# Kernel optimization log

Hardware: AMD Instinct MI355X
Metric: run time of the kernel (lower is better)

The kernel has to match this reference:

```python
import jax, jax.numpy as jnp
import numpy as np

NUM_ITERS = 3

def squash(s, axis=-1):
    # standard capsule squash: ||s||^2/(1+||s||^2) * s/||s||
    sq = jnp.sum(s * s, axis=axis, keepdims=True)
    norm = jnp.sqrt(sq)
    return (sq / (1.0 + sq)) * (s / norm)

def setup_inputs() -> dict:
    key = jax.random.key(0)
    kx, kw = jax.random.split(key)
    B, I, k, l, O = 512, 1152, 8, 16, 7
    x = jax.random.normal(kx, (B, I, k), dtype=jnp.float32)
    w = jax.random.normal(kw, (I, k, l, O), dtype=jnp.float32)
    return {"x": x, "w": w}

def reference(x, w):
    # x: [B, I, k]; w: [I, k, l, O]
    u_hat = jnp.einsum('BIk,IklO->BIlO', x, w)            # [B, I, l, O]
    I, _, l, _ = w.shape
    b_ij = jnp.zeros((I, l), dtype=u_hat.dtype)
    v_j = None
    for _ in range(NUM_ITERS):
        c_ij = jax.nn.softmax(b_ij, axis=0)               # softmax over I
        s_j = jnp.einsum('Il,BIlO->BlO', c_ij, u_hat)     # [B, l, O]
        v_j = jnp.transpose(squash(s_j), (0, 2, 1))       # [B, O, l]
        u_vj = jnp.einsum('BOl,BIlO->BIl', v_j, u_hat).mean(axis=0)  # [I, l]
        b_ij = b_ij + u_vj
    return v_j
```

## Files before the change

### kernel.cpp

```cpp
#include <hip/hip_runtime.h>
#include <hip/hip_bf16.h>


#define NB 512
#define NI 1152
#define NLO 112
#define NIK 9216
#define NPAD 128

typedef __attribute__((ext_vector_type(8))) short bf16x8;
typedef __attribute__((ext_vector_type(4))) float f32x4;

__device__ __forceinline__ ushort f2bf(float f) {
    __hip_bfloat16 h = __float2bfloat16(f);
    return *(ushort*)&h;
}
__device__ __forceinline__ float bf2f(short s) {
    union { unsigned int u; float f; } v;
    v.u = ((unsigned int)(unsigned short)s) << 16;
    return v.f;
}

__device__ __forceinline__ void conv_x_body(const float* __restrict__ x,
                                            ushort* __restrict__ xbf,
                                            ushort* __restrict__ xT, int bid) {
    __shared__ ushort tile[64][68];
    int kg = bid % 144, bg = bid / 144;
    int k0 = kg * 64, b0 = bg * 64;
    int t = threadIdx.x;
    for (int e = t; e < 1024; e += 256) {
        int r = e >> 4, c4 = (e & 15) * 4;
        float4 f = *(const float4*)&x[(size_t)(b0 + r) * NIK + k0 + c4];
        ushort4 u = { f2bf(f.x), f2bf(f.y), f2bf(f.z), f2bf(f.w) };
        *(ushort4*)&xbf[(size_t)(b0 + r) * NIK + k0 + c4] = u;
        tile[r][c4] = u.x; tile[r][c4 + 1] = u.y; tile[r][c4 + 2] = u.z; tile[r][c4 + 3] = u.w;
    }
    __syncthreads();
    for (int e = t; e < 1024; e += 256) {
        int kr = e >> 4, c4 = (e & 15) * 4;
        ushort4 u = { tile[c4][kr], tile[c4 + 1][kr], tile[c4 + 2][kr], tile[c4 + 3][kr] };
        *(ushort4*)&xT[(size_t)(k0 + kr) * NB + b0 + c4] = u;
    }
}

__global__ __launch_bounds__(256) void prep0(const float* __restrict__ x,
                                             ushort* __restrict__ xbf,
                                             ushort* __restrict__ xT,
                                             const float* __restrict__ w,
                                             ushort* __restrict__ wpT,
                                             ushort* __restrict__ wps,
                                             float* __restrict__ Z) {
    if (blockIdx.x < 1152) { conv_x_body(x, xbf, xT, blockIdx.x); return; }
    __shared__ ushort tile[NPAD][66];
    int t = threadIdx.x;
    int wb = blockIdx.x - 1152;
    int ik0 = wb * 64;
    if (blockIdx.x == 1152 && t < 48) Z[t] = (t < 16) ? 1152.0f : 0.0f;
    for (int e = t; e < 8192; e += 256) {
        int ikl = e >> 7, np = e & 127;
        int l = np >> 3, o = np & 7;
        float wv = (o < 7) ? w[(size_t)(ik0 + ikl) * NLO + l * 7 + o] : 0.f;
        tile[np][ikl] = f2bf(wv);
    }
    __syncthreads();
    for (int e = t; e < 8192; e += 256) {
        int np = e >> 6, ikl = e & 63;
        ushort v = tile[np][ikl];
        wpT[(size_t)np * NIK + ik0 + ikl] = v;
        wps[(size_t)np * NIK + ik0 + ikl] = v;
    }
}

__global__ __launch_bounds__(1024) void sq_gemm(const ushort* __restrict__ xbf,
                                                const ushort* __restrict__ wps,
                                                const float* __restrict__ Zit,
                                                ushort* __restrict__ vT,
                                                float* __restrict__ out, int wout) {
    __shared__ float sp[16][16][16];
    __shared__ float ss[16][16];
    __shared__ float facs[16][2];
    __shared__ float zi[2];
    int bid = blockIdx.x;
    int mt = bid & 31, ng = bid >> 5;
    int b0 = mt * 16, n0 = ng * 16;
    int t = threadIdx.x;
    int wv = t >> 6, lane = t & 63;
    int row = lane & 15, quad = lane >> 4;
    int k0 = wv * 576;
    if (t < 2) zi[t] = 1.0f / Zit[ng * 2 + t];
    const ushort* ap = xbf + (size_t)(b0 + row) * NIK + k0 + quad * 8;
    const ushort* bp = wps + (size_t)(n0 + row) * NIK + k0 + quad * 8;
    f32x4 acc = {0.f, 0.f, 0.f, 0.f};
    #pragma unroll
    for (int ks = 0; ks < 18; ++ks) {
        bf16x8 a = *(const bf16x8*)(ap + ks * 32);
        bf16x8 b = *(const bf16x8*)(bp + ks * 32);
        acc = __builtin_amdgcn_mfma_f32_16x16x32_bf16(a, b, acc, 0, 0, 0);
    }
    #pragma unroll
    for (int r = 0; r < 4; ++r) sp[wv][quad * 4 + r][row] = acc[r];
    __syncthreads();
    if (t < 256) {
        int m = t >> 4, n = t & 15;
        float sv = 0.f;
        #pragma unroll
        for (int w8 = 0; w8 < 16; ++w8) sv += sp[w8][m][n];
        ss[m][n] = sv * zi[n >> 3];
    }
    __syncthreads();
    if (t < 32) {
        int m = t >> 1, ll = t & 1;
        float sq = 0.f;
        #pragma unroll
        for (int o = 0; o < 8; ++o) { float e = ss[m][ll * 8 + o]; sq += e * e; }
        facs[m][ll] = sqrtf(sq) / (1.0f + sq);
    }
    __syncthreads();
    if (t < 256) {
        int m = t >> 4, n = t & 15;
        int o = n & 7, lg = ng * 2 + (n >> 3);
        if (o < 7) {
            float vv = ss[m][n] * facs[m][n >> 3];
            vT[(size_t)(o * 16 + lg) * NB + b0 + m] = f2bf(vv);
            if (wout) out[(size_t)(b0 + m) * NLO + o * 16 + lg] = vv;
        }
    }
}

__global__ __launch_bounds__(512) void g_wc(const ushort* __restrict__ xT,
                                            const ushort* __restrict__ vT,
                                            const float* __restrict__ w,
                                            float* __restrict__ bij,
                                            const ushort* __restrict__ wpT,
                                            ushort* __restrict__ wps,
                                            float* __restrict__ Zit, int accum) {
    __shared__ float bs[2][8][16];
    __shared__ float cs[128];
    int t = threadIdx.x;
    int wv = t >> 6;
    int lane = t & 63;
    int half = wv & 1;
    int mt = wv >> 1;
    int m0 = blockIdx.x * 64 + mt * 16;
    int kb0 = half * 256;
    int row = lane & 15, quad = lane >> 4;
    const ushort* ap = xT + (size_t)(m0 + row) * NB + kb0 + quad * 8;
    const ushort* bp = vT + (size_t)row * NB + kb0 + quad * 8;
    f32x4 acc[7];
    #pragma unroll
    for (int nt = 0; nt < 7; ++nt) acc[nt] = (f32x4){0.f, 0.f, 0.f, 0.f};
    #pragma unroll
    for (int ks = 0; ks < 8; ++ks) {
        bf16x8 a = *(const bf16x8*)(ap + ks * 32);
        #pragma unroll
        for (int nt = 0; nt < 7; ++nt) {
            bf16x8 bfr = *(const bf16x8*)(bp + (size_t)nt * 16 * NB + ks * 32);
            acc[nt] = __builtin_amdgcn_mfma_f32_16x16x32_bf16(a, bfr, acc[nt], 0, 0, 0);
        }
    }
    float S = 0.f;
    #pragma unroll
    for (int r = 0; r < 4; ++r) {
        int ik = m0 + quad * 4 + r;
        const float* wr = w + (size_t)ik * NLO + row * 7;
        float p = 0.f;
        #pragma unroll
        for (int o = 0; o < 7; ++o) p += wr[o] * acc[o][r];
        S += p;
    }
    float Sp = __shfl_down(S, 16);
    if ((quad & 1) == 0)
        bs[half][mt * 2 + (quad >> 1)][row] = (S + Sp) * (1.0f / 512.0f);
    __syncthreads();
    if (t < 128) {
        int il = t >> 4, l = t & 15;
        int i = blockIdx.x * 8 + il;
        float val = bs[0][il][l] + bs[1][il][l];
        if (accum) val += bij[i * 16 + l];
        bij[i * 16 + l] = val;
        cs[t] = expf(val);
    }
    __syncthreads();
    if (t < 16) {
        float z = 0.f;
        #pragma unroll
        for (int j = 0; j < 8; ++j) z += cs[j * 16 + t];
        atomicAdd(&Zit[t], z);
    }
    int ik0 = blockIdx.x * 64;
    for (int e = t; e < 2048; e += 512) {
        int np = e >> 4, i4 = (e & 15) * 4;
        float sc = cs[(i4 >> 3) * 16 + (np >> 3)];
        ushort4 wv4 = *(const ushort4*)&wpT[(size_t)np * NIK + ik0 + i4];
        ushort4 o4 = { f2bf(bf2f((short)wv4.x) * sc), f2bf(bf2f((short)wv4.y) * sc),
                       f2bf(bf2f((short)wv4.z) * sc), f2bf(bf2f((short)wv4.w) * sc) };
        *(ushort4*)&wps[(size_t)np * NIK + ik0 + i4] = o4;
    }
}

extern "C" void kernel_launch(void* const* d_in, const int* in_sizes, int n_in,
                              void* d_out, int out_size, void* d_ws, size_t ws_size,
                              hipStream_t stream) {
    const float* x = (const float*)d_in[0];
    const float* w = (const float*)d_in[1];
    float* out = (float*)d_out;
    float* ws = (float*)d_ws;
    float*  f_bij  = ws;
    float*  f_Z    = f_bij + NI * 16;
    ushort* xbf    = (ushort*)(f_Z + 48);
    ushort* xT     = xbf + (size_t)NB * NIK;
    ushort* wpT    = xT + (size_t)NIK * NB;
    ushort* wps    = wpT + (size_t)NPAD * NIK;
    ushort* vT     = wps + (size_t)NPAD * NIK;
    prep0<<<1296, 256, 0, stream>>>(x, xbf, xT, w, wpT, wps, f_Z);
    for (int it = 0; it < 3; ++it) {
        sq_gemm<<<256, 1024, 0, stream>>>(xbf, wps, f_Z + it * 16, vT, out,
                                          it == 2 ? 1 : 0);
        if (it < 2)
            g_wc<<<144, 512, 0, stream>>>(xT, vT, w, f_bij, wpT, wps,
                                          f_Z + (it + 1) * 16, it);
    }
}
```

Baseline: 174.1 us.

## Fuse routing iterations into one cooperative kernel with grid-wide syncs

Replaces the five separate sq_gemm/g_wc launches with a single cooperative kernel that loops over the three routing iterations and uses grid.sync() between phases. The agreement GEMM phase now runs on 144 of the 256 blocks with 1024 threads, splitting K into four quarters instead of two. This removes per-launch overhead and gaps between small kernels, in exchange for grid-wide barrier cost and idle blocks during the agreement phase.

Measured after the change: 314.4 us. +80.6%, slower.

```diff
diff --git a/kernel.cpp b/kernel.cpp
--- a/kernel.cpp
+++ b/kernel.cpp
@@ -1,5 +1,8 @@
 #include <hip/hip_runtime.h>
 #include <hip/hip_bf16.h>
+#include <hip/hip_cooperative_groups.h>
+
+namespace cg = cooperative_groups;
 
 
 #define NB 512
@@ -71,130 +74,131 @@
     }
 }
 
-__global__ __launch_bounds__(1024) void sq_gemm(const ushort* __restrict__ xbf,
-                                                const ushort* __restrict__ wps,
-                                                const float* __restrict__ Zit,
-                                                ushort* __restrict__ vT,
-                                                float* __restrict__ out, int wout) {
+__global__ __launch_bounds__(1024, 4) void route(const ushort* __restrict__ xbf,
+                                                 ushort* __restrict__ wps,
+                                                 float* __restrict__ Z,
+                                                 ushort* __restrict__ vT,
+                                                 float* __restrict__ out,
+                                                 const ushort* __restrict__ xT,
+                                                 const float* __restrict__ w,
+                                                 float* __restrict__ bij,
+                                                 const ushort* __restrict__ wpT) {
+    cg::grid_group grid = cg::this_grid();
     __shared__ float sp[16][16][16];
     __shared__ float ss[16][16];
     __shared__ float facs[16][2];
     __shared__ float zi[2];
+    __shared__ float bs[4][8][16];
+    __shared__ float cs[128];
     int bid = blockIdx.x;
-    int mt = bid & 31, ng = bid >> 5;
-    int b0 = mt * 16, n0 = ng * 16;
     int t = threadIdx.x;
     int wv = t >> 6, lane = t & 63;
     int row = lane & 15, quad = lane >> 4;
+    int mt = bid & 31, ng = bid >> 5;
+    int b0 = mt * 16, n0 = ng * 16;
     int k0 = wv * 576;
-    if (t < 2) zi[t] = 1.0f / Zit[ng * 2 + t];
     const ushort* ap = xbf + (size_t)(b0 + row) * NIK + k0 + quad * 8;
     const ushort* bp = wps + (size_t)(n0 + row) * NIK + k0 + quad * 8;
-    f32x4 acc = {0.f, 0.f, 0.f, 0.f};
-    #pragma unroll
-    for (int ks = 0; ks < 18; ++ks) {
-        bf16x8 a = *(const bf16x8*)(ap + ks * 32);
-        bf16x8 b = *(const bf16x8*)(bp + ks * 32);
-        acc = __builtin_amdgcn_mfma_f32_16x16x32_bf16(a, b, acc, 0, 0, 0);
-    }
-    #pragma unroll
-    for (int r = 0; r < 4; ++r) sp[wv][quad * 4 + r][row] = acc[r];
-    __syncthreads();
-    if (t < 256) {
-        int m = t >> 4, n = t & 15;
-        float sv = 0.f;
+
+    for (int it = 0; it < 3; ++it) {
+        if (t < 2) zi[t] = 1.0f / Z[it * 16 + ng * 2 + t];
+        f32x4 acc = {0.f, 0.f, 0.f, 0.f};
         #pragma unroll
-        for (int w8 = 0; w8 < 16; ++w8) sv += sp[w8][m][n];
-        ss[m][n] = sv * zi[n >> 3];
-    }
-    __syncthreads();
-    if (t < 32) {
-        int m = t >> 1, ll = t & 1;
-        float sq = 0.f;
+        for (int ks = 0; ks < 18; ++ks) {
+            bf16x8 a = *(const bf16x8*)(ap + ks * 32);
+            bf16x8 b = *(const bf16x8*)(bp + ks * 32);
+            acc = __builtin_amdgcn_mfma_f32_16x16x32_bf16(a, b, acc, 0, 0, 0);
+        }
         #pragma unroll
-        for (int o = 0; o < 8; ++o) { float e = ss[m][ll * 8 + o]; sq += e * e; }
-        facs[m][ll] = sqrtf(sq) / (1.0f + sq);
-    }
-    __syncthreads();
-    if (t < 256) {
-        int m = t >> 4, n = t & 15;
-        int o = n & 7, lg = ng * 2 + (n >> 3);
-        if (o < 7) {
-            float vv = ss[m][n] * facs[m][n >> 3];
-            vT[(size_t)(o * 16 + lg) * NB + b0 + m] = f2bf(vv);
-            if (wout) out[(size_t)(b0 + m) * NLO + o * 16 + lg] = vv;
-        }
-    }
-}
-
-__global__ __launch_bounds__(512) void g_wc(const ushort* __restrict__ xT,
-                                            const ushort* __restrict__ vT,
-                                            const float* __restrict__ w,
-                                            float* __restrict__ bij,
-                                            const ushort* __restrict__ wpT,
-                                            ushort* __restrict__ wps,
-                                            float* __restrict__ Zit, int accum) {
-    __shared__ float bs[2][8][16];
-    __shared__ float cs[128];
-    int t = threadIdx.x;
-    int wv = t >> 6;
-    int lane = t & 63;
-    int half = wv & 1;
-    int mt = wv >> 1;
-    int m0 = blockIdx.x * 64 + mt * 16;
-    int kb0 = half * 256;
-    int row = lane & 15, quad = lane >> 4;
-    const ushort* ap = xT + (size_t)(m0 + row) * NB + kb0 + quad * 8;
-    const ushort* bp = vT + (size_t)row * NB + kb0 + quad * 8;
-    f32x4 acc[7];
-    #pragma unroll
-    for (int nt = 0; nt < 7; ++nt) acc[nt] = (f32x4){0.f, 0.f, 0.f, 0.f};
-    #pragma unroll
-    for (int ks = 0; ks < 8; ++ks) {
-        bf16x8 a = *(const bf16x8*)(ap + ks * 32);
-        #pragma unroll
-        for (int nt = 0; nt < 7; ++nt) {
-            bf16x8 bfr = *(const bf16x8*)(bp + (size_t)nt * 16 * NB + ks * 32);
-            acc[nt] = __builtin_amdgcn_mfma_f32_16x16x32_bf16(a, bfr, acc[nt], 0, 0, 0);
-        }
-    }
-    float S = 0.f;
-    #pragma unroll
-    for (int r = 0; r < 4; ++r) {
-        int ik = m0 + quad * 4 + r;
-        const float* wr = w + (size_t)ik * NLO + row * 7;
-        float p = 0.f;
-        #pragma unroll
-        for (int o = 0; o < 7; ++o) p += wr[o] * acc[o][r];
-        S += p;
-    }
-    float Sp = __shfl_down(S, 16);
-    if ((quad & 1) == 0)
-        bs[half][mt * 2 + (quad >> 1)][row] = (S + Sp) * (1.0f / 512.0f);
-    __syncthreads();
-    if (t < 128) {
-        int il = t >> 4, l = t & 15;
-        int i = blockIdx.x * 8 + il;
-        float val = bs[0][il][l] + bs[1][il][l];
-        if (accum) val += bij[i * 16 + l];
-        bij[i * 16 + l] = val;
-        cs[t] = expf(val);
-    }
-    __syncthreads();
-    if (t < 16) {
-        float z = 0.f;
-        #pragma unroll
-        for (int j = 0; j < 8; ++j) z += cs[j * 16 + t];
-        atomicAdd(&Zit[t], z);
-    }
-    int ik0 = blockIdx.x * 64;
-    for (int e = t; e < 2048; e += 512) {
-        int np = e >> 4, i4 = (e & 15) * 4;
-        float sc = cs[(i4 >> 3) * 16 + (np >> 3)];
-        ushort4 wv4 = *(const ushort4*)&wpT[(size_t)np * NIK + ik0 + i4];
-        ushort4 o4 = { f2bf(bf2f((short)wv4.x) * sc), f2bf(bf2f((short)wv4.y) * sc),
-                       f2bf(bf2f((short)wv4.z) * sc), f2bf(bf2f((short)wv4.w) * sc) };
-        *(ushort4*)&wps[(size_t)np * NIK + ik0 + i4] = o4;
+        for (int r = 0; r < 4; ++r) sp[wv][quad * 4 + r][row] = acc[r];
+        __syncthreads();
+        if (t < 256) {
+            int m = t >> 4, n = t & 15;
+            float sv = 0.f;
+            #pragma unroll
+            for (int w8 = 0; w8 < 16; ++w8) sv += sp[w8][m][n];
+            ss[m][n] = sv * zi[n >> 3];
+        }
+        __syncthreads();
+        if (t < 32) {
+            int m = t >> 1, ll = t & 1;
+            float sq = 0.f;
+            #pragma unroll
+            for (int o = 0; o < 8; ++o) { float e = ss[m][ll * 8 + o]; sq += e * e; }
+            facs[m][ll] = sqrtf(sq) / (1.0f + sq);
+        }
+        __syncthreads();
+        if (t < 256) {
+            int m = t >> 4, n = t & 15;
+            int o = n & 7, lg = ng * 2 + (n >> 3);
+            if (o < 7) {
+                float vv = ss[m][n] * facs[m][n >> 3];
+                vT[(size_t)(o * 16 + lg) * NB + b0 + m] = f2bf(vv);
+                if (it == 2) out[(size_t)(b0 + m) * NLO + o * 16 + lg] = vv;
+            }
+        }
+        if (it == 2) break;
+        grid.sync();
+
+        if (bid < 144) {
+            int qt = wv & 3;
+            int mtg = wv >> 2;
+            int m0 = bid * 64 + mtg * 16;
+            int kb0 = qt * 128;
+            const ushort* gap = xT + (size_t)(m0 + row) * NB + kb0 + quad * 8;
+            const ushort* gbp = vT + (size_t)row * NB + kb0 + quad * 8;
+            f32x4 gacc[7];
+            #pragma unroll
+            for (int nt = 0; nt < 7; ++nt) gacc[nt] = (f32x4){0.f, 0.f, 0.f, 0.f};
+            #pragma unroll
+            for (int ks = 0; ks < 4; ++ks) {
+                bf16x8 a = *(const bf16x8*)(gap + ks * 32);
+                #pragma unroll
+                for (int nt = 0; nt < 7; ++nt) {
+                    bf16x8 bfr = *(const bf16x8*)(gbp + (size_t)nt * 16 * NB + ks * 32);
+                    gacc[nt] = __builtin_amdgcn_mfma_f32_16x16x32_bf16(a, bfr, gacc[nt], 0, 0, 0);
+                }
+            }
+            float S = 0.f;
+            #pragma unroll
+            for (int r = 0; r < 4; ++r) {
+                int ik = m0 + quad * 4 + r;
+                const float* wr = w + (size_t)ik * NLO + row * 7;
+                float p = 0.f;
+                #pragma unroll
+                for (int o = 0; o < 7; ++o) p += wr[o] * gacc[o][r];
+                S += p;
+            }
+            float Sp = __shfl_down(S, 16);
+            if ((quad & 1) == 0)
+                bs[qt][mtg * 2 + (quad >> 1)][row] = (S + Sp) * (1.0f / 512.0f);
+            __syncthreads();
+            if (t < 128) {
+                int il = t >> 4, l = t & 15;
+                int i = bid * 8 + il;
+                float val = bs[0][il][l] + bs[1][il][l] + bs[2][il][l] + bs[3][il][l];
+                if (it) val += bij[i * 16 + l];
+                bij[i * 16 + l] = val;
+                cs[t] = expf(val);
+            }
+            __syncthreads();
+            if (t < 16) {
+                float z = 0.f;
+                #pragma unroll
+                for (int j = 0; j < 8; ++j) z += cs[j * 16 + t];
+                atomicAdd(&Z[(it + 1) * 16 + t], z);
+            }
+            int ik0 = bid * 64;
+            for (int e = t; e < 2048; e += 1024) {
+                int np = e >> 4, i4 = (e & 15) * 4;
+                float sc = cs[(i4 >> 3) * 16 + (np >> 3)];
+                ushort4 wv4 = *(const ushort4*)&wpT[(size_t)np * NIK + ik0 + i4];
+                ushort4 o4 = { f2bf(bf2f((short)wv4.x) * sc), f2bf(bf2f((short)wv4.y) * sc),
+                               f2bf(bf2f((short)wv4.z) * sc), f2bf(bf2f((short)wv4.w) * sc) };
+                *(ushort4*)&wps[(size_t)np * NIK + ik0 + i4] = o4;
+            }
+        }
+        grid.sync();
     }
 }
 
@@ -213,11 +217,12 @@
     ushort* wps    = wpT + (size_t)NPAD * NIK;
     ushort* vT     = wps + (size_t)NPAD * NIK;
     prep0<<<1296, 256, 0, stream>>>(x, xbf, xT, w, wpT, wps, f_Z);
-    for (int it = 0; it < 3; ++it) {
-        sq_gemm<<<256, 1024, 0, stream>>>(xbf, wps, f_Z + it * 16, vT, out,
-                                          it == 2 ? 1 : 0);
-        if (it < 2)
-            g_wc<<<144, 512, 0, stream>>>(xT, vT, w, f_bij, wpT, wps,
-                                          f_Z + (it + 1) * 16, it);
-    }
-}
+    const ushort* xbf_c = xbf;
+    const ushort* xT_c = xT;
+    const ushort* wpT_c = wpT;
+    void* args[] = { (void*)&xbf_c, (void*)&wps, (void*)&f_Z, (void*)&vT,
+                     (void*)&out, (void*)&xT_c, (void*)&w, (void*)&f_bij,
+                     (void*)&wpT_c };
+    hipLaunchCooperativeKernel((const void*)route, dim3(256), dim3(1024),
+                               args, 0, stream);
+}
```
